# Kernel tuning notes

Hardware: AMD Instinct MI355X
Metric: run time of the kernel (lower is better)

## Reference

```python
import jax, jax.numpy as jnp
import numpy as np

HEADS = 16
DIM_HEAD = 64
LN_EPS = 1e-3  # keras LayerNormalization default


def setup_inputs() -> dict:
    key = jax.random.key(0)
    ks = jax.random.split(key, 4)
    B, N, D = 8, 512, 1024
    inner = HEADS * DIM_HEAD  # 1024
    return {
        "x": jax.random.normal(ks[0], (B, N, D), dtype=jnp.float32),
        "w_qkv": jax.random.normal(ks[1], (D, 3 * inner), dtype=jnp.float32) * (D ** -0.5),
        "reattn_w": jax.random.normal(ks[2], (HEADS, HEADS), dtype=jnp.float32),
        "ln_gamma": jnp.ones((HEADS,), dtype=jnp.float32),
        "ln_beta": jnp.zeros((HEADS,), dtype=jnp.float32),
        "w_out": jax.random.normal(ks[3], (inner, D), dtype=jnp.float32) * (inner ** -0.5),
        "b_out": jnp.zeros((D,), dtype=jnp.float32),
    }


def reference(x, w_qkv, reattn_w, ln_gamma, ln_beta, w_out, b_out):
    B, N, D = x.shape
    H, dh = HEADS, DIM_HEAD
    scale = dh ** -0.5

    qkv = x @ w_qkv  # [B, N, 3*H*dh]
    q, k, v = jnp.split(qkv, 3, axis=-1)
    # b n (h d) -> b h n d
    to_heads = lambda t: t.reshape(B, N, H, dh).transpose(0, 2, 1, 3)
    q, k, v = to_heads(q), to_heads(k), to_heads(v)

    dots = jnp.einsum("bhid,bhjd->bhij", q, k) * scale  # [B, H, N, N]
    attn = jax.nn.softmax(dots, axis=-1)

    # re-attention: mix across heads
    attn = jnp.einsum("bhij,hg->bgij", attn, reattn_w)

    # LayerNorm over the head axis (axis=1), keras default eps
    mean = jnp.mean(attn, axis=1, keepdims=True)
    var = jnp.var(attn, axis=1, keepdims=True)
    attn = (attn - mean) * jax.lax.rsqrt(var + LN_EPS)
    attn = attn * ln_gamma[None, :, None, None] + ln_beta[None, :, None, None]

    out = jnp.einsum("bhij,bhjd->bhid", attn, v)  # [B, H, N, dh]
    out = out.transpose(0, 2, 1, 3).reshape(B, N, H * dh)  # b h n d -> b n (h d)
    return out @ w_out + b_out
```

## Files before the change

kernel.cpp:

```cpp
#include <hip/hip_runtime.h>
#include <math.h>

#define BB 8
#define NN 512
#define DD 1024
#define HH 16
#define DH 64
#define INNER 1024
#define QKV3 3072
#define PSTR (NN * NN + 64)

typedef __attribute__((ext_vector_type(8))) short short8;
typedef __attribute__((ext_vector_type(4))) float f32x4;

#define AS1 __attribute__((address_space(1)))
#define AS3 __attribute__((address_space(3)))

__device__ __forceinline__ float4 ld4(const float* p) { return *(const float4*)p; }

__device__ __forceinline__ unsigned short f2bf(float f) {
    unsigned u = __float_as_uint(f);
    return (unsigned short)((u + 0x7fffu + ((u >> 16) & 1u)) >> 16);
}
__device__ __forceinline__ float bf2f(unsigned short u) {
    return __uint_as_float(((unsigned)u) << 16);
}

__global__ void conv_bf16(const float* __restrict__ in, unsigned short* __restrict__ out) {
    size_t i = ((size_t)blockIdx.x * 256 + threadIdx.x) * 4;
    float4 v = ld4(in + i);
    ushort4 o;
    o.x = f2bf(v.x); o.y = f2bf(v.y); o.z = f2bf(v.z); o.w = f2bf(v.w);
    *(ushort4*)(out + i) = o;
}

__global__ void convT_bf16(const float* __restrict__ in, unsigned short* __restrict__ out,
                           int K, int N) {
    __shared__ float t[32][33];
    const int n0 = blockIdx.x * 32, k0 = blockIdx.y * 32;
    const int tx = threadIdx.x & 31, ty = threadIdx.x >> 5;
#pragma unroll
    for (int l = 0; l < 4; ++l)
        t[ty + 8 * l][tx] = in[(size_t)(k0 + ty + 8 * l) * N + n0 + tx];
    __syncthreads();
#pragma unroll
    for (int l = 0; l < 4; ++l)
        out[(size_t)(n0 + ty + 8 * l) * K + k0 + tx] = f2bf(t[tx][ty + 8 * l]);
}

__global__ __launch_bounds__(256) void gemm_bf16(
    const unsigned short* __restrict__ A, const unsigned short* __restrict__ Bt,
    float* __restrict__ C, const float* __restrict__ bias, int M, int N, int K) {
    __shared__ short As[128 * 32];
    __shared__ short Bs[128 * 32];
    const int tid = threadIdx.x;
    const int w = tid >> 6, l = tid & 63;
    const int bm = blockIdx.y * 128, bn = blockIdx.x * 128;
    const int wm = (w >> 1) * 64, wn = (w & 1) * 64;
    const int lrow = l & 15, lq = l >> 4;

    f32x4 acc[4][4];
#pragma unroll
    for (int i = 0; i < 4; ++i)
#pragma unroll
        for (int j = 0; j < 4; ++j) acc[i][j] = (f32x4){0.f, 0.f, 0.f, 0.f};

    for (int k0 = 0; k0 < K; k0 += 32) {
#pragma unroll
        for (int t = 0; t < 2; ++t) {
            const int q = w * 2 + t;
            const int li = q * 512 + l * 8;
            const int row = li >> 5, kc = li & 31;
            const unsigned short* ga = A + (size_t)(bm + row) * K + k0 + kc;
            __builtin_amdgcn_global_load_lds(
                (const AS1 void*)ga, (AS3 void*)(As + q * 512), 16, 0, 0);
            const unsigned short* gb = Bt + (size_t)(bn + row) * K + k0 + kc;
            __builtin_amdgcn_global_load_lds(
                (const AS1 void*)gb, (AS3 void*)(Bs + q * 512), 16, 0, 0);
        }
        __syncthreads();

        short8 a[4], b[4];
#pragma unroll
        for (int i = 0; i < 4; ++i)
            a[i] = *(const short8*)(As + (wm + i * 16 + lrow) * 32 + lq * 8);
#pragma unroll
        for (int j = 0; j < 4; ++j)
            b[j] = *(const short8*)(Bs + (wn + j * 16 + lrow) * 32 + lq * 8);
#pragma unroll
        for (int i = 0; i < 4; ++i)
#pragma unroll
            for (int j = 0; j < 4; ++j)
                acc[i][j] = __builtin_amdgcn_mfma_f32_16x16x32_bf16(a[i], b[j], acc[i][j], 0, 0, 0);
        __syncthreads();
    }

#pragma unroll
    for (int i = 0; i < 4; ++i)
#pragma unroll
        for (int j = 0; j < 4; ++j) {
            const int col = bn + wn + j * 16 + lrow;
            const float bv = bias ? bias[col] : 0.f;
#pragma unroll
            for (int r = 0; r < 4; ++r) {
                const int row = bm + wm + i * 16 + lq * 4 + r;
                C[(size_t)row * N + col] = acc[i][j][r] + bv;
            }
        }
}

__global__ __launch_bounds__(256) void gemm_bf16_bf(
    const unsigned short* __restrict__ A, const unsigned short* __restrict__ Bt,
    unsigned short* __restrict__ C, int M, int N, int K) {
    __shared__ short As[128 * 32];
    __shared__ short Bs[128 * 32];
    const int tid = threadIdx.x;
    const int w = tid >> 6, l = tid & 63;
    const int bm = blockIdx.y * 128, bn = blockIdx.x * 128;
    const int wm = (w >> 1) * 64, wn = (w & 1) * 64;
    const int lrow = l & 15, lq = l >> 4;

    f32x4 acc[4][4];
#pragma unroll
    for (int i = 0; i < 4; ++i)
#pragma unroll
        for (int j = 0; j < 4; ++j) acc[i][j] = (f32x4){0.f, 0.f, 0.f, 0.f};

    for (int k0 = 0; k0 < K; k0 += 32) {
#pragma unroll
        for (int t = 0; t < 2; ++t) {
            const int q = w * 2 + t;
            const int li = q * 512 + l * 8;
            const int row = li >> 5, kc = li & 31;
            const unsigned short* ga = A + (size_t)(bm + row) * K + k0 + kc;
            __builtin_amdgcn_global_load_lds(
                (const AS1 void*)ga, (AS3 void*)(As + q * 512), 16, 0, 0);
            const unsigned short* gb = Bt + (size_t)(bn + row) * K + k0 + kc;
            __builtin_amdgcn_global_load_lds(
                (const AS1 void*)gb, (AS3 void*)(Bs + q * 512), 16, 0, 0);
        }
        __syncthreads();

        short8 a[4], b[4];
#pragma unroll
        for (int i = 0; i < 4; ++i)
            a[i] = *(const short8*)(As + (wm + i * 16 + lrow) * 32 + lq * 8);
#pragma unroll
        for (int j = 0; j < 4; ++j)
            b[j] = *(const short8*)(Bs + (wn + j * 16 + lrow) * 32 + lq * 8);
#pragma unroll
        for (int i = 0; i < 4; ++i)
#pragma unroll
            for (int j = 0; j < 4; ++j)
                acc[i][j] = __builtin_amdgcn_mfma_f32_16x16x32_bf16(a[i], b[j], acc[i][j], 0, 0, 0);
        __syncthreads();
    }

#pragma unroll
    for (int i = 0; i < 4; ++i)
#pragma unroll
        for (int j = 0; j < 4; ++j) {
            const int col = bn + wn + j * 16 + lrow;
#pragma unroll
            for (int r = 0; r < 4; ++r) {
                const int row = bm + wm + i * 16 + lq * 4 + r;
                C[(size_t)row * N + col] = f2bf(acc[i][j][r]);
            }
        }
}

__global__ __launch_bounds__(256) void scores_stream(
    const unsigned short* __restrict__ qkvb, unsigned short* __restrict__ attnb,
    float* __restrict__ lsum2) {
    const int bh = blockIdx.z;
    const int h = bh & 15, b = bh >> 4;
    const int jh = blockIdx.y;
    const int w = threadIdx.x >> 6, l = threadIdx.x & 63;
    const int i0 = blockIdx.x * 64 + w * 16;
    const int lrow = l & 15, lq = l >> 4;

    const unsigned short* qb = qkvb + (size_t)(b * NN) * QKV3 + h * DH + lq * 8;
    const unsigned short* kb = qkvb + (size_t)(b * NN) * QKV3 + INNER + h * DH + lq * 8;

    const short8 qf0 = *(const short8*)(qb + (size_t)(i0 + lrow) * QKV3);
    const short8 qf1 = *(const short8*)(qb + (size_t)(i0 + lrow) * QKV3 + 32);

    const unsigned short* krow = kb + (size_t)(jh * 256 + lrow) * QKV3;
    unsigned short* orow = attnb + (size_t)bh * PSTR + (size_t)(i0 + lrow) * NN +
                           jh * 256 + lq * 4;

    short8 ka[4], kc[4];
#pragma unroll
    for (int p = 0; p < 4; ++p) {
        const unsigned short* kp = krow + (size_t)p * 16 * QKV3;
        ka[p] = *(const short8*)(kp);
        kc[p] = *(const short8*)(kp + 32);
    }

    float lacc = 0.f;
#pragma unroll
    for (int jt = 0; jt < 16; ++jt) {
        const int s = jt & 3;
        short8 kf0 = ka[s], kf1 = kc[s];
        if (jt < 12) {
            const unsigned short* kp = krow + (size_t)(jt + 4) * 16 * QKV3;
            ka[s] = *(const short8*)(kp);
            kc[s] = *(const short8*)(kp + 32);
        }
        f32x4 acc = (f32x4){0.f, 0.f, 0.f, 0.f};
        acc = __builtin_amdgcn_mfma_f32_16x16x32_bf16(kf0, qf0, acc, 0, 0, 0);
        acc = __builtin_amdgcn_mfma_f32_16x16x32_bf16(kf1, qf1, acc, 0, 0, 0);
        float e0 = __expf(acc[0] * 0.125f);
        float e1 = __expf(acc[1] * 0.125f);
        float e2 = __expf(acc[2] * 0.125f);
        float e3 = __expf(acc[3] * 0.125f);
        lacc += (e0 + e1) + (e2 + e3);
        ushort4 o;
        o.x = f2bf(e0); o.y = f2bf(e1); o.z = f2bf(e2); o.w = f2bf(e3);
        *(ushort4*)(orow + jt * 16) = o;
    }
    lacc += __shfl_xor(lacc, 16, 64);
    lacc += __shfl_xor(lacc, 32, 64);
    if (lq == 0)
        lsum2[(size_t)jh * BB * HH * NN + (size_t)bh * NN + i0 + lrow] = lacc;
}

__global__ void reattn_ln_bf(unsigned short* __restrict__ attnb,
                             const float* __restrict__ lsum2,
                             const float* __restrict__ rw,
                             const float* __restrict__ gamma,
                             const float* __restrict__ beta) {
    __shared__ float w[16][16];
    __shared__ float gs[16], bs[16];
    const int tid = threadIdx.x;
    ((float*)w)[tid] = rw[tid];
    if (tid < 16) { gs[tid] = gamma[tid]; bs[tid] = beta[tid]; }
    __syncthreads();

    const size_t idx = (size_t)blockIdx.x * 256 + tid;
    const int j4 = (int)(idx & 127);
    const int i = (int)((idx >> 7) & 511);
    const int b = (int)(idx >> 16);
    unsigned short* base = attnb + (size_t)(b * HH) * PSTR + (size_t)i * NN + j4 * 4;
    const float* l0 = lsum2 + (size_t)(b * HH) * NN + i;
    const float* l1 = l0 + (size_t)BB * HH * NN;

    float v[16][4];
#pragma unroll
    for (int h = 0; h < 16; ++h) {
        const float linv = 1.0f / (l0[h * NN] + l1[h * NN]);
        ushort4 u = *(const ushort4*)(base + (size_t)h * PSTR);
        v[h][0] = bf2f(u.x) * linv; v[h][1] = bf2f(u.y) * linv;
        v[h][2] = bf2f(u.z) * linv; v[h][3] = bf2f(u.w) * linv;
    }
    float o[16][4];
    float me[4] = {0.f, 0.f, 0.f, 0.f};
#pragma unroll
    for (int g = 0; g < 16; ++g) {
        float s0 = 0.f, s1 = 0.f, s2 = 0.f, s3 = 0.f;
#pragma unroll
        for (int h = 0; h < 16; ++h) {
            const float wg = w[h][g];
            s0 += v[h][0] * wg; s1 += v[h][1] * wg;
            s2 += v[h][2] * wg; s3 += v[h][3] * wg;
        }
        o[g][0] = s0; o[g][1] = s1; o[g][2] = s2; o[g][3] = s3;
        me[0] += s0; me[1] += s1; me[2] += s2; me[3] += s3;
    }
#pragma unroll
    for (int r = 0; r < 4; ++r) me[r] *= 0.0625f;
    float va[4] = {0.f, 0.f, 0.f, 0.f};
#pragma unroll
    for (int g = 0; g < 16; ++g)
#pragma unroll
        for (int r = 0; r < 4; ++r) {
            float d = o[g][r] - me[r];
            va[r] += d * d;
        }
    float ri[4];
#pragma unroll
    for (int r = 0; r < 4; ++r) ri[r] = rsqrtf(va[r] * 0.0625f + 1e-3f);
#pragma unroll
    for (int g = 0; g < 16; ++g) {
        ushort4 u;
        u.x = f2bf((o[g][0] - me[0]) * ri[0] * gs[g] + bs[g]);
        u.y = f2bf((o[g][1] - me[1]) * ri[1] * gs[g] + bs[g]);
        u.z = f2bf((o[g][2] - me[2]) * ri[2] * gs[g] + bs[g]);
        u.w = f2bf((o[g][3] - me[3]) * ri[3] * gs[g] + bs[g]);
        *(ushort4*)(base + (size_t)g * PSTR) = u;
    }
}

__global__ void transpose_v(const unsigned short* __restrict__ qkvb,
                            unsigned short* __restrict__ vT) {
    __shared__ unsigned short t[32][33];
    const int bh = blockIdx.z;
    const int h = bh & 15, b = bh >> 4;
    const int j0 = blockIdx.x * 32, d0 = blockIdx.y * 32;
    const int tx = threadIdx.x & 31, ty = threadIdx.x >> 5;
    const unsigned short* src = qkvb + (size_t)(b * NN) * QKV3 + 2 * INNER + h * DH;
#pragma unroll
    for (int k = 0; k < 4; ++k)
        t[ty + 8 * k][tx] = src[(size_t)(j0 + ty + 8 * k) * QKV3 + d0 + tx];
    __syncthreads();
    unsigned short* dst = vT + (size_t)bh * DH * NN;
#pragma unroll
    for (int k = 0; k < 4; ++k)
        dst[(size_t)(d0 + ty + 8 * k) * NN + j0 + tx] = t[tx][ty + 8 * k];
}

__global__ __launch_bounds__(256) void pv_mfma(
    const unsigned short* __restrict__ attnb, const unsigned short* __restrict__ vT,
    unsigned short* __restrict__ outhb) {
    const int bh = blockIdx.y;
    const int h = bh & 15, b = bh >> 4;
    const int i0 = blockIdx.x * 128;
    __shared__ short Ps[128 * 64];
    __shared__ short Vs[64 * 64];
    const int tid = threadIdx.x;
    const int w = tid >> 6, l = tid & 63;
    const int lrow = l & 15, lq = l >> 4;
    const int lr8 = l >> 3;
    const int swd = ((l & 7) ^ (lr8 & 7)) * 8;

    f32x4 acc[2][4];
#pragma unroll
    for (int ic = 0; ic < 2; ++ic)
#pragma unroll
        for (int dt = 0; dt < 4; ++dt) acc[ic][dt] = (f32x4){0.f, 0.f, 0.f, 0.f};

    const unsigned short* pb = attnb + (size_t)bh * PSTR + (size_t)i0 * NN;
    const unsigned short* vb = vT + (size_t)bh * DH * NN;

    for (int j0 = 0; j0 < NN; j0 += 64) {
#pragma unroll
        for (int t = 0; t < 4; ++t) {
            int c = w * 4 + t;
            int r = c * 8 + lr8;
            __builtin_amdgcn_global_load_lds(
                (const AS1 void*)(pb + (size_t)r * NN + j0 + swd),
                (AS3 void*)(Ps + c * 512), 16, 0, 0);
        }
#pragma unroll
        for (int t = 0; t < 2; ++t) {
            int c = w * 2 + t;
            int d = c * 8 + lr8;
            __builtin_amdgcn_global_load_lds(
                (const AS1 void*)(vb + (size_t)d * NN + j0 + swd),
                (AS3 void*)(Vs + c * 512), 16, 0, 0);
        }
        __syncthreads();

#pragma unroll
        for (int kh = 0; kh < 2; ++kh) {
            short8 vf[4];
#pragma unroll
            for (int dt = 0; dt < 4; ++dt)
                vf[dt] = *(const short8*)(Vs + (dt * 16 + lrow) * 64 + (((kh * 4 + lq) ^ (lrow & 7)) * 8));
#pragma unroll
            for (int ic = 0; ic < 2; ++ic) {
                short8 pf = *(const short8*)(Ps + (w * 32 + ic * 16 + lrow) * 64 + (((kh * 4 + lq) ^ (lrow & 7)) * 8));
#pragma unroll
                for (int dt = 0; dt < 4; ++dt)
                    acc[ic][dt] = __builtin_amdgcn_mfma_f32_16x16x32_bf16(vf[dt], pf, acc[ic][dt], 0, 0, 0);
            }
        }
        __syncthreads();
    }

#pragma unroll
    for (int ic = 0; ic < 2; ++ic) {
        unsigned short* orow = outhb +
            ((size_t)(b * NN + i0 + w * 32 + ic * 16 + lrow)) * INNER + h * DH + lq * 4;
#pragma unroll
        for (int dt = 0; dt < 4; ++dt) {
            ushort4 o;
            o.x = f2bf(acc[ic][dt][0]); o.y = f2bf(acc[ic][dt][1]);
            o.z = f2bf(acc[ic][dt][2]); o.w = f2bf(acc[ic][dt][3]);
            *(ushort4*)(orow + dt * 16) = o;
        }
    }
}

extern "C" void kernel_launch(void* const* d_in, const int* in_sizes, int n_in,
                              void* d_out, int out_size, void* d_ws, size_t ws_size,
                              hipStream_t stream) {
    const float* x        = (const float*)d_in[0];
    const float* w_qkv    = (const float*)d_in[1];
    const float* reattn_w = (const float*)d_in[2];
    const float* ln_gamma = (const float*)d_in[3];
    const float* ln_beta  = (const float*)d_in[4];
    const float* w_out    = (const float*)d_in[5];
    const float* b_out    = (const float*)d_in[6];
    float* out = (float*)d_out;

    unsigned short* qkvb  = (unsigned short*)d_ws;
    unsigned short* attnb = qkvb + (size_t)BB * NN * QKV3;
    unsigned short* vTb   = attnb + (size_t)BB * HH * PSTR;
    unsigned short* outhb = vTb + (size_t)BB * HH * DH * NN;
    unsigned short* xb    = outhb + (size_t)BB * NN * INNER;
    unsigned short* wqkvT = xb + (size_t)BB * NN * DD;
    unsigned short* woutT = wqkvT + (size_t)DD * QKV3;
    float*          lsum2 = (float*)(woutT + (size_t)INNER * INNER);

    dim3 blk(256);

    conv_bf16<<<dim3((BB * NN * DD) / 1024), blk, 0, stream>>>(x, xb);
    convT_bf16<<<dim3(QKV3 / 32, DD / 32), blk, 0, stream>>>(w_qkv, wqkvT, DD, QKV3);
    convT_bf16<<<dim3(INNER / 32, INNER / 32), blk, 0, stream>>>(w_out, woutT, INNER, INNER);

    gemm_bf16_bf<<<dim3(QKV3 / 128, (BB * NN) / 128), blk, 0, stream>>>(
        xb, wqkvT, qkvb, BB * NN, QKV3, DD);

    scores_stream<<<dim3(NN / 64, 2, BB * HH), blk, 0, stream>>>(qkvb, attnb, lsum2);

    reattn_ln_bf<<<dim3((BB * NN * NN) / 1024), blk, 0, stream>>>(
        attnb, lsum2, reattn_w, ln_gamma, ln_beta);

    transpose_v<<<dim3(NN / 32, DH / 32, BB * HH), blk, 0, stream>>>(qkvb, vTb);

    pv_mfma<<<dim3(NN / 128, BB * HH), blk, 0, stream>>>(attnb, vTb, outhb);

    gemm_bf16<<<dim3(INNER / 128, (BB * NN) / 128), blk, 0, stream>>>(
        outhb, woutT, out, b_out, BB * NN, INNER, INNER);
}
```

Baseline: 245.3 us.

## Replace QKV GEMM with 256x256 tile, double-buffered, swizzled LDS pipeline

Rewrites the QKV projection GEMM to use 256x256 output tiles with 512 threads. It double-buffers A and B tiles in LDS through async global-to-LDS loads interleaved with the MFMA phases, and XOR-swizzles LDS offsets to avoid bank conflicts. The aim is to hide global load latency behind matrix math and raise data reuse per tile. In exchange the kernel gets much more complex, with hand-placed waitcnt and barriers and heavy register use for 32 accumulators per lane. The grid also shrinks to 192 blocks, which may underfill the GPU.

```diff
diff --git a/kernel.cpp b/kernel.cpp
--- a/kernel.cpp
+++ b/kernel.cpp
@@ -109,62 +109,101 @@
         }
 }
 
-__global__ __launch_bounds__(256) void gemm_bf16_bf(
+__device__ __forceinline__ void stage_st(const unsigned short* __restrict__ G, int K,
+                                         int row0, int kt, short* dst_half,
+                                         int w, int l) {
+    const int grow = row0 + w * 16 + (l >> 2);
+    const int gcol = kt * 32 + (((l & 3) * 8) ^ ((l & 32) ? 16 : 0));
+    __builtin_amdgcn_global_load_lds(
+        (const AS1 void*)(G + (size_t)grow * K + gcol),
+        (AS3 void*)(dst_half + w * 512), 16, 0, 0);
+}
+
+__global__ __launch_bounds__(512, 2) void gemm256_bf(
     const unsigned short* __restrict__ A, const unsigned short* __restrict__ Bt,
     unsigned short* __restrict__ C, int M, int N, int K) {
-    __shared__ short As[128 * 32];
-    __shared__ short Bs[128 * 32];
+    __shared__ __align__(16) short lds_[2 * 16384];
     const int tid = threadIdx.x;
     const int w = tid >> 6, l = tid & 63;
-    const int bm = blockIdx.y * 128, bn = blockIdx.x * 128;
-    const int wm = (w >> 1) * 64, wn = (w & 1) * 64;
+    const int wm = w >> 2, wn = w & 3;
     const int lrow = l & 15, lq = l >> 4;
-
-    f32x4 acc[4][4];
-#pragma unroll
-    for (int i = 0; i < 4; ++i)
+    const int bm = blockIdx.y * 256, bn = blockIdx.x * 256;
+    const int NT = K >> 5;
+
+    const int aoff = lrow * 32 + ((lq * 8) ^ ((lrow & 8) ? 16 : 0));
+    const int bsub = (wn & 1) * 4;
+
+    f32x4 acc[8][4];
+#pragma unroll
+    for (int i = 0; i < 8; ++i)
 #pragma unroll
         for (int j = 0; j < 4; ++j) acc[i][j] = (f32x4){0.f, 0.f, 0.f, 0.f};
 
-    for (int k0 = 0; k0 < K; k0 += 32) {
-#pragma unroll
-        for (int t = 0; t < 2; ++t) {
-            const int q = w * 2 + t;
-            const int li = q * 512 + l * 8;
-            const int row = li >> 5, kc = li & 31;
-            const unsigned short* ga = A + (size_t)(bm + row) * K + k0 + kc;
-            __builtin_amdgcn_global_load_lds(
-                (const AS1 void*)ga, (AS3 void*)(As + q * 512), 16, 0, 0);
-            const unsigned short* gb = Bt + (size_t)(bn + row) * K + k0 + kc;
-            __builtin_amdgcn_global_load_lds(
-                (const AS1 void*)gb, (AS3 void*)(Bs + q * 512), 16, 0, 0);
-        }
-        __syncthreads();
-
-        short8 a[4], b[4];
-#pragma unroll
-        for (int i = 0; i < 4; ++i)
-            a[i] = *(const short8*)(As + (wm + i * 16 + lrow) * 32 + lq * 8);
-#pragma unroll
-        for (int j = 0; j < 4; ++j)
-            b[j] = *(const short8*)(Bs + (wn + j * 16 + lrow) * 32 + lq * 8);
-#pragma unroll
-        for (int i = 0; i < 4; ++i)
-#pragma unroll
-            for (int j = 0; j < 4; ++j)
-                acc[i][j] = __builtin_amdgcn_mfma_f32_16x16x32_bf16(a[i], b[j], acc[i][j], 0, 0, 0);
-        __syncthreads();
-    }
-
-#pragma unroll
-    for (int i = 0; i < 4; ++i)
-#pragma unroll
-        for (int j = 0; j < 4; ++j) {
-            const int col = bn + wn + j * 16 + lrow;
+    stage_st(A,  K, bm,       0, lds_ + 0,                    w, l);
+    stage_st(A,  K, bm + 128, 0, lds_ + 4096,                 w, l);
+    stage_st(Bt, K, bn,       0, lds_ + 8192,                 w, l);
+    stage_st(Bt, K, bn + 128, 0, lds_ + 8192 + 4096,          w, l);
+    stage_st(Bt, K, bn,       1, lds_ + 16384 + 8192,         w, l);
+    stage_st(Bt, K, bn + 128, 1, lds_ + 16384 + 8192 + 4096,  w, l);
+    asm volatile("s_waitcnt vmcnt(2)" ::: "memory");
+    __builtin_amdgcn_s_barrier();
+
+    for (int t = 0; t < NT; ++t) {
+        const int s = t & 1;
+        const short* Ah = lds_ + s * 16384 + wm * 4096;
+        const short* Bh = lds_ + s * 16384 + 8192 + (wn >> 1) * 4096;
+        short8 bfr[4];
+#pragma unroll
+        for (int p = 0; p < 4; ++p) {
+            short8 a0 = *(const short8*)(Ah + (2 * p) * 512 + aoff);
+            short8 a1 = *(const short8*)(Ah + (2 * p + 1) * 512 + aoff);
+            if (p == 0) {
+#pragma unroll
+                for (int fc = 0; fc < 4; ++fc)
+                    bfr[fc] = *(const short8*)(Bh + (bsub + fc) * 512 + aoff);
+            }
+            if (p == 0 && t + 1 < NT)
+                stage_st(A,  K, bm,       t + 1, lds_ + (s ^ 1) * 16384,               w, l);
+            if (p == 1 && t + 1 < NT)
+                stage_st(A,  K, bm + 128, t + 1, lds_ + (s ^ 1) * 16384 + 4096,        w, l);
+            if (p == 2 && t + 2 < NT)
+                stage_st(Bt, K, bn,       t + 2, lds_ + s * 16384 + 8192,              w, l);
+            if (p == 3 && t + 2 < NT)
+                stage_st(Bt, K, bn + 128, t + 2, lds_ + s * 16384 + 8192 + 4096,       w, l);
+
+            __builtin_amdgcn_s_barrier();
+            asm volatile("s_waitcnt lgkmcnt(0)" ::: "memory");
+            __builtin_amdgcn_sched_barrier(0);
+
+            __builtin_amdgcn_s_setprio(1);
+#pragma unroll
+            for (int fc = 0; fc < 4; ++fc) {
+                acc[2 * p][fc] =
+                    __builtin_amdgcn_mfma_f32_16x16x32_bf16(a0, bfr[fc], acc[2 * p][fc], 0, 0, 0);
+                acc[2 * p + 1][fc] =
+                    __builtin_amdgcn_mfma_f32_16x16x32_bf16(a1, bfr[fc], acc[2 * p + 1][fc], 0, 0, 0);
+            }
+            __builtin_amdgcn_s_setprio(0);
+
+            if (p == 3) {
+                if (t == NT - 2)
+                    asm volatile("s_waitcnt vmcnt(0)" ::: "memory");
+                else if (t < NT - 2)
+                    asm volatile("s_waitcnt vmcnt(2)" ::: "memory");
+            }
+            __builtin_amdgcn_s_barrier();
+        }
+    }
+
+#pragma unroll
+    for (int fr = 0; fr < 8; ++fr)
+#pragma unroll
+        for (int fc = 0; fc < 4; ++fc) {
+            const int col = bn + wn * 64 + fc * 16 + lrow;
 #pragma unroll
             for (int r = 0; r < 4; ++r) {
-                const int row = bm + wm + i * 16 + lq * 4 + r;
-                C[(size_t)row * N + col] = f2bf(acc[i][j][r]);
+                const int row = bm + wm * 128 + fr * 16 + lq * 4 + r;
+                C[(size_t)row * N + col] = f2bf(acc[fr][fc][r]);
             }
         }
 }
@@ -409,7 +448,7 @@
     convT_bf16<<<dim3(QKV3 / 32, DD / 32), blk, 0, stream>>>(w_qkv, wqkvT, DD, QKV3);
     convT_bf16<<<dim3(INNER / 32, INNER / 32), blk, 0, stream>>>(w_out, woutT, INNER, INNER);
 
-    gemm_bf16_bf<<<dim3(QKV3 / 128, (BB * NN) / 128), blk, 0, stream>>>(
+    gemm256_bf<<<dim3(QKV3 / 256, (BB * NN) / 256), dim3(512), 0, stream>>>(
         xb, wqkvT, qkvb, BB * NN, QKV3, DD);
 
     scores_stream<<<dim3(NN / 64, 2, BB * HH), blk, 0, stream>>>(qkvb, attnb, lsum2);
```

Result: no change. 244.1 us (-0.5%).
